# Performance work log

Hardware: AMD Instinct MI355X
Metric: run time of the kernel (lower is better)

The kernel has to match this reference:

```python
import jax, jax.numpy as jnp
import numpy as np

B, T, HID = 2, 2048, 1024
H, D = 16, 64
ROPE = 32
GIDX = (2, 3, 4, 5)
MASK_VAL = -1e9


def setup_inputs() -> dict:
    key = jax.random.key(0)
    ks = jax.random.split(key, 5)
    x = jax.random.normal(ks[0], (B, T, HID), jnp.float32)
    mask = jnp.triu(jnp.ones((T, T), jnp.bool_), 1)  # True above diagonal -> masked (causal)
    qkv_w = jax.random.normal(ks[1], (3 * H * D, HID), jnp.float32) * (1.0 / np.sqrt(HID))
    qkv_b = jax.random.normal(ks[2], (3 * H * D,), jnp.float32) * 0.02
    out_w = jax.random.normal(ks[3], (HID, H * D), jnp.float32) * (1.0 / np.sqrt(H * D))
    out_b = jax.random.normal(ks[4], (HID,), jnp.float32) * 0.02
    return {"x": x, "mask": mask, "qkv_w": qkv_w, "qkv_b": qkv_b, "out_w": out_w, "out_b": out_b}


def _rope_tables(t):
    inv_freq = 1.0 / (10000.0 ** (jnp.arange(0, ROPE, 2, dtype=jnp.float32) / ROPE))
    freqs = jnp.arange(t, dtype=jnp.float32)[:, None] * inv_freq[None, :]  # [T, ROPE/2]
    return jnp.cos(freqs), jnp.sin(freqs)


def _apply_rotary(x, cos, sin):
    # x: [B,H,T,D]; rotate first ROPE dims as interleaved pairs
    xr = x[..., :ROPE].reshape(*x.shape[:-1], ROPE // 2, 2)
    x1, x2 = xr[..., 0], xr[..., 1]
    rot = jnp.stack([x1 * cos - x2 * sin, x1 * sin + x2 * cos], axis=-1).reshape(*x.shape[:-1], ROPE)
    return jnp.concatenate([rot, x[..., ROPE:]], axis=-1)


def reference(x, mask, qkv_w, qkv_b, out_w, out_b):
    b, t, _ = x.shape
    qkv = x @ qkv_w.T + qkv_b                      # [B,T,3*H*D]
    q, k, v = jnp.split(qkv, 3, axis=-1)
    q, k, v = [y.reshape(b, t, H, D).transpose(0, 2, 1, 3) for y in (q, k, v)]  # [B,H,T,D]
    cos, sin = _rope_tables(t)                      # [T, ROPE/2] broadcast over B,H
    q = _apply_rotary(q, cos, sin)
    k = _apply_rotary(k, cos, sin)
    scale = 1.0 / np.sqrt(D)
    # local dense causal attention
    scores = jnp.einsum('bhqd,bhkd->bhqk', q, k) * scale
    scores = jnp.where(mask, MASK_VAL, scores)
    out_local = jnp.einsum('bhqk,bhkd->bhqd', jax.nn.softmax(scores, axis=-1), v)
    # global token pass with its own causal overlay
    gidx = jnp.array(GIDX)
    gq = q[:, :, gidx]                              # [B,H,G,D]
    gs = jnp.einsum('bhgd,bhkd->bhgk', gq, k) * scale
    gmask = jnp.arange(t)[None, :] > gidx[:, None]  # [G,T]: col > row -> masked
    gs = jnp.where(gmask, MASK_VAL, gs)
    gout = jnp.einsum('bhgk,bhkd->bhgd', jax.nn.softmax(gs, axis=-1), v)
    out = out_local.at[:, :, gidx].set(gout)
    attn_out = out.transpose(0, 2, 1, 3).reshape(b, t, H * D)
    return attn_out @ out_w.T + out_b
```

## Files before the change

### kernel.cpp

```cpp
#include <hip/hip_runtime.h>
#include <math.h>

typedef unsigned short u16;
typedef unsigned int u32;
typedef __attribute__((ext_vector_type(4))) float f32x4;
typedef __attribute__((ext_vector_type(8))) short bf16x8;

#define B_ 2
#define T_ 2048
#define H_ 16
#define HID 1024
#define NQKV 3072
#define M_ 4096
#define SCALE_Q 0.18033688011112042f

__device__ __forceinline__ u16 f2bf(float f) {
  union { float f; unsigned u; } v; v.f = f;
  unsigned r = v.u + 0x7FFFu + ((v.u >> 16) & 1u);
  return (u16)(r >> 16);
}
__device__ __forceinline__ float bf2f(u16 u) {
  union { unsigned u; float f; } v; v.u = ((unsigned)u) << 16; return v.f;
}
__device__ __forceinline__ u32 cvt_pk_bf16(float lo, float hi) {
  u32 r;
  asm("v_cvt_pk_bf16_f32 %0, %1, %2" : "=v"(r) : "v"(lo), "v"(hi));
  return r;
}
__device__ __forceinline__ float fexp2(float x) { return __builtin_amdgcn_exp2f(x); }

__device__ __forceinline__ void gload16(const void* g, void* l) {
  __builtin_amdgcn_global_load_lds((const __attribute__((address_space(1))) void*)g,
                                   (__attribute__((address_space(3))) void*)l, 16, 0, 0);
}

__global__ void prep(const float* __restrict__ x, const float* __restrict__ qkv_w,
                     const float* __restrict__ out_w, u16* __restrict__ xb,
                     u16* __restrict__ wqkv, u16* __restrict__ wout, float* __restrict__ tab) {
  int bid = blockIdx.x;
  if (bid < 128) {
    int i = bid * 256 + threadIdx.x;
    int tpos = i >> 4, f = i & 15;
    float ang = (float)tpos * exp2f(-(float)f * 0.83048202372184058696f);
    float s, c;
    sincosf(ang, &s, &c);
    tab[i * 2] = c;
    tab[i * 2 + 1] = s;
    return;
  }
  bid -= 128;
  const float* in;
  u16* out;
  if (bid < 4096) { in = x; out = xb; }
  else if (bid < 7168) { bid -= 4096; in = qkv_w; out = wqkv; }
  else { bid -= 7168; in = out_w; out = wout; }
  int i = bid * 256 + threadIdx.x;
  float4 v = ((const float4*)in)[i];
  uint2 o;
  o.x = (unsigned)f2bf(v.x) | ((unsigned)f2bf(v.y) << 16);
  o.y = (unsigned)f2bf(v.z) | ((unsigned)f2bf(v.w) << 16);
  ((uint2*)out)[i] = o;
}

__global__ __launch_bounds__(256) void gemm_qkv(const u16* __restrict__ A,
    const u16* __restrict__ Bt, const float* __restrict__ bias, const float* __restrict__ tab,
    u16* __restrict__ Q, u16* __restrict__ K, u16* __restrict__ Vt)
{
  __shared__ u16 lsA[2][128 * 32];
  __shared__ u16 lsB[2][128 * 32];
  const int t = threadIdx.x;
  const int l = t & 63, w = t >> 6;
  const int wm = (w >> 1) * 64, wn = (w & 1) * 64;
  const int lr = l & 15, lg = l >> 4;
  const long bm = (long)blockIdx.y * 128, bn = (long)blockIdx.x * 128;
  const int KD = HID;

  f32x4 acc[4][4];
#pragma unroll
  for (int i = 0; i < 4; i++)
#pragma unroll
    for (int j = 0; j < 4; j++) acc[i][j] = (f32x4){0.f, 0.f, 0.f, 0.f};

  const int srow = l >> 2, sko = (l & 3) * 8;
  const u16* Ab = A + (bm + srow) * (long)KD + sko;
  const u16* Bb = Bt + (bn + srow) * (long)KD + sko;

  auto stage = [&](int buf, int k0) {
#pragma unroll
    for (int g = 0; g < 2; g++)
      gload16(Ab + (long)((w * 2 + g) * 16) * KD + k0, &lsA[buf][(w * 2 + g) * 512]);
#pragma unroll
    for (int g = 0; g < 2; g++)
      gload16(Bb + (long)((w * 2 + g) * 16) * KD + k0, &lsB[buf][(w * 2 + g) * 512]);
  };

  stage(0, 0);
  __syncthreads();
  int cur = 0;
  for (int k0 = 0; k0 < KD; k0 += 32) {
    if (k0 + 32 < KD) stage(cur ^ 1, k0 + 32);
    bf16x8 af[4], bfv[4];
#pragma unroll
    for (int mi = 0; mi < 4; mi++)
      af[mi] = *(const bf16x8*)&lsA[cur][(wm + mi * 16 + lr) * 32 + lg * 8];
#pragma unroll
    for (int ni = 0; ni < 4; ni++)
      bfv[ni] = *(const bf16x8*)&lsB[cur][(wn + ni * 16 + lr) * 32 + lg * 8];
    __builtin_amdgcn_s_setprio(1);
#pragma unroll
    for (int mi = 0; mi < 4; mi++)
#pragma unroll
      for (int ni = 0; ni < 4; ni++)
        acc[mi][ni] = __builtin_amdgcn_mfma_f32_16x16x32_bf16(af[mi], bfv[ni], acc[mi][ni], 0, 0, 0);
    __builtin_amdgcn_s_setprio(0);
    __syncthreads();
    cur ^= 1;
  }

  const int region = (int)(bn >> 10);
  const int h = (int)(((bn + wn) & 1023) >> 6);
  const float2* tab2 = (const float2*)tab;
  u16* QK = (region == 0) ? Q : K;

#pragma unroll
  for (int mi = 0; mi < 4; mi++) {
    const int m0 = (int)(bm) + wm + mi * 16 + lg * 4;
    const int b = m0 >> 11, t0 = m0 & (T_ - 1);
    const long bh = b * 16 + h;
#pragma unroll
    for (int ni = 0; ni < 4; ni++) {
      const int d = ni * 16 + lr;
      const long col = bn + wn + d;
      const float bv = bias[col];
      float vv[4];
#pragma unroll
      for (int r = 0; r < 4; r++) vv[r] = acc[mi][ni][r] + bv;
      if (region < 2 && ni < 2) {
        const int fi = d >> 1;
        const float sgn = (d & 1) ? 1.f : -1.f;
#pragma unroll
        for (int r = 0; r < 4; r++) {
          float pvv = __shfl_xor(vv[r], 1, 64);
          float2 cs = tab2[(t0 + r) * 16 + fi];
          vv[r] = vv[r] * cs.x + sgn * pvv * cs.y;
        }
      }
      if (region == 0) {
#pragma unroll
        for (int r = 0; r < 4; r++) vv[r] *= SCALE_Q;
      }
      if (region < 2) {
#pragma unroll
        for (int r = 0; r < 4; r++)
          QK[(bh * T_ + t0 + r) * 64 + d] = f2bf(vv[r]);
      } else {
        uint2 pk;
        pk.x = cvt_pk_bf16(vv[0], vv[1]);
        pk.y = cvt_pk_bf16(vv[2], vv[3]);
        *(uint2*)&Vt[(bh * 64 + d) * (long)T_ + t0] = pk;
      }
    }
  }
}

__global__ __launch_bounds__(256) void gemm_out(const u16* __restrict__ A,
    const u16* __restrict__ Bt, const float* __restrict__ bias,
    float* __restrict__ outp, int N, int K)
{
  constexpr int BM = 64;
  constexpr int MI = 4, NI = 2;
  __shared__ u16 lsA[2][BM * 32];
  __shared__ u16 lsB[2][128 * 32];
  const int t = threadIdx.x;
  const int l = t & 63, w = t >> 6;
  const int wn = w * 32;
  const int lr = l & 15, lg = l >> 4;
  const long bm = (long)blockIdx.y * BM, bn = (long)blockIdx.x * 128;

  f32x4 acc[MI][NI];
#pragma unroll
  for (int i = 0; i < MI; i++)
#pragma unroll
    for (int j = 0; j < NI; j++) acc[i][j] = (f32x4){0.f, 0.f, 0.f, 0.f};

  const int srow = l >> 2, sko = (l & 3) * 8;
  const u16* Ab = A + (bm + srow) * (long)K + sko;
  const u16* Bb = Bt + (bn + srow) * (long)K + sko;

  auto stage = [&](int buf, int k0) {
    gload16(Ab + (long)(w * 16) * K + k0, &lsA[buf][w * 512]);
    gload16(Bb + (long)(w * 16) * K + k0, &lsB[buf][w * 512]);
    gload16(Bb + (long)((w + 4) * 16) * K + k0, &lsB[buf][(w + 4) * 512]);
  };

  stage(0, 0);
  __syncthreads();
  int cur = 0;
  for (int k0 = 0; k0 < K; k0 += 32) {
    if (k0 + 32 < K) stage(cur ^ 1, k0 + 32);
    bf16x8 af[MI], bfv[NI];
#pragma unroll
    for (int mi = 0; mi < MI; mi++)
      af[mi] = *(const bf16x8*)&lsA[cur][(mi * 16 + lr) * 32 + lg * 8];
#pragma unroll
    for (int ni = 0; ni < NI; ni++)
      bfv[ni] = *(const bf16x8*)&lsB[cur][(wn + ni * 16 + lr) * 32 + lg * 8];
    __builtin_amdgcn_s_setprio(1);
#pragma unroll
    for (int mi = 0; mi < MI; mi++)
#pragma unroll
      for (int ni = 0; ni < NI; ni++)
        acc[mi][ni] = __builtin_amdgcn_mfma_f32_16x16x32_bf16(af[mi], bfv[ni], acc[mi][ni], 0, 0, 0);
    __builtin_amdgcn_s_setprio(0);
    __syncthreads();
    cur ^= 1;
  }
#pragma unroll
  for (int mi = 0; mi < MI; mi++)
#pragma unroll
    for (int ni = 0; ni < NI; ni++) {
      long row = bm + mi * 16 + lg * 4;
      long col = bn + wn + ni * 16 + lr;
      float bv = bias[col];
#pragma unroll
      for (int r = 0; r < 4; r++)
        outp[(row + r) * (long)N + col] = acc[mi][ni][r] + bv;
    }
}

__global__ __launch_bounds__(256, 4) void fattn(const u16* __restrict__ Q, const u16* __restrict__ Kp,
                                                const u16* __restrict__ V, u16* __restrict__ O) {
  const int id = blockIdx.x;
  const int qt = 31 - (id >> 5);
  const int bh = id & 31;
  __shared__ u16 lsK[2][64 * 64];
  __shared__ u16 lsV[2][64 * 64];
  __shared__ u32 lsP[4][16 * 36];
  const int t = threadIdx.x, l = t & 63, w = t >> 6;
  const int lr = l & 15, lg = l >> 4;
  const u16* Qb = Q + (long)bh * T_ * 64;
  const u16* Kb = Kp + (long)bh * T_ * 64;
  const u16* Vb = V + (long)bh * 64 * T_;
  u32* lsPw = lsP[w];

  bf16x8 aq[2];
#pragma unroll
  for (int ks = 0; ks < 2; ks++)
    aq[ks] = *(const bf16x8*)&Qb[((long)(qt * 64 + w * 16 + lr)) * 64 + ks * 32 + lg * 8];

  f32x4 o[4];
#pragma unroll
  for (int di = 0; di < 4; di++) o[di] = (f32x4){0.f, 0.f, 0.f, 0.f};
  float mrow = -1e30f, lrow = 0.f;

  const int srow = l >> 3;
  const int scx = ((l & 7) ^ srow) * 8;
  const long kgo0 = (long)(16 * w + srow) * 64 + scx;
  const long kgo1 = (long)(16 * w + 8 + srow) * 64 + scx;
  const long vgo0 = (long)(16 * w + srow) * T_ + scx;
  const long vgo1 = (long)(16 * w + 8 + srow) * T_ + scx;

  gload16(Kb + kgo0, &lsK[0][(2 * w) * 512]);
  gload16(Kb + kgo1, &lsK[0][(2 * w + 1) * 512]);
  gload16(Vb + vgo0, &lsV[0][(2 * w) * 512]);
  gload16(Vb + vgo1, &lsV[0][(2 * w + 1) * 512]);
  __syncthreads();

  int cur = 0;
  for (int kt = 0; kt <= qt; kt++) {
    if (kt < qt) {
      const u16* kp = Kb + (kt + 1) * 4096;
      const u16* vp = Vb + (kt + 1) * 64;
      gload16(kp + kgo0, &lsK[cur ^ 1][(2 * w) * 512]);
      gload16(kp + kgo1, &lsK[cur ^ 1][(2 * w + 1) * 512]);
      gload16(vp + vgo0, &lsV[cur ^ 1][(2 * w) * 512]);
      gload16(vp + vgo1, &lsV[cur ^ 1][(2 * w + 1) * 512]);
    }

    f32x4 s[4];
#pragma unroll
    for (int ji = 0; ji < 4; ji++) s[ji] = (f32x4){0.f, 0.f, 0.f, 0.f};
    __builtin_amdgcn_s_setprio(1);
#pragma unroll
    for (int ks = 0; ks < 2; ks++)
#pragma unroll
      for (int ji = 0; ji < 4; ji++) {
        int row = ji * 16 + lr;
        bf16x8 kf = *(const bf16x8*)&lsK[cur][row * 64 + ((ks * 32 + lg * 8) ^ ((row & 7) * 8))];
        s[ji] = __builtin_amdgcn_mfma_f32_16x16x32_bf16(kf, aq[ks], s[ji], 0, 0, 0);
      }
    __builtin_amdgcn_s_setprio(0);

    if (kt == qt) {
      int qloc = w * 16 + lr;
#pragma unroll
      for (int ji = 0; ji < 4; ji++)
#pragma unroll
        for (int r = 0; r < 4; r++)
          if (ji * 16 + lg * 4 + r > qloc) s[ji][r] = -1e30f;
    }

    float mx = s[0][0];
#pragma unroll
    for (int ji = 0; ji < 4; ji++)
#pragma unroll
      for (int r = 0; r < 4; r++) mx = fmaxf(mx, s[ji][r]);
    mx = fmaxf(mx, __shfl_xor(mx, 16, 64));
    mx = fmaxf(mx, __shfl_xor(mx, 32, 64));

    if (__any(mx - mrow > 8.f)) {
      float newm = fmaxf(mrow, mx);
      float sf = fexp2(mrow - newm);
      mrow = newm;
      lrow *= sf;
#pragma unroll
      for (int r = 0; r < 4; r++) {
        float sfb = __shfl(sf, lg * 4 + r, 64);
#pragma unroll
        for (int di = 0; di < 4; di++) o[di][r] *= sfb;
      }
    }

    float rs = 0.f;
    u32 pd[8];
#pragma unroll
    for (int ji = 0; ji < 4; ji++)
#pragma unroll
      for (int hh = 0; hh < 2; hh++) {
        float p0 = fexp2(s[ji][2 * hh] - mrow);
        float p1 = fexp2(s[ji][2 * hh + 1] - mrow);
        rs += p0 + p1;
        pd[ji * 2 + hh] = cvt_pk_bf16(p0, p1);
      }
    rs += __shfl_xor(rs, 16, 64);
    rs += __shfl_xor(rs, 32, 64);
    lrow += rs;

#pragma unroll
    for (int ji = 0; ji < 4; ji++)
      *(uint2*)&lsPw[lr * 36 + ji * 8 + lg * 2] = make_uint2(pd[2 * ji], pd[2 * ji + 1]);
    __builtin_amdgcn_s_setprio(1);
#pragma unroll
    for (int js = 0; js < 2; js++) {
      bf16x8 pa = *(const bf16x8*)&lsPw[lr * 36 + js * 16 + lg * 4];
#pragma unroll
      for (int di = 0; di < 4; di++) {
        int drow = di * 16 + lr;
        bf16x8 vb = *(const bf16x8*)&lsV[cur][drow * 64 + ((js * 32 + lg * 8) ^ ((drow & 7) * 8))];
        o[di] = __builtin_amdgcn_mfma_f32_16x16x32_bf16(pa, vb, o[di], 0, 0, 0);
      }
    }
    __builtin_amdgcn_s_setprio(0);

    if (kt < qt) __syncthreads();
    cur ^= 1;
  }

  const int b = bh >> 4, h = bh & 15;
  float inv = 1.f / lrow;
#pragma unroll
  for (int r = 0; r < 4; r++) {
    float invb = __shfl(inv, lg * 4 + r, 64);
#pragma unroll
    for (int di = 0; di < 4; di++) {
      long rowt = (long)(b * T_ + qt * 64 + w * 16 + lg * 4 + r);
      O[rowt * 1024 + h * 64 + di * 16 + lr] = f2bf(o[di][r] * invb);
    }
  }
}

extern "C" void kernel_launch(void* const* d_in, const int* in_sizes, int n_in,
                              void* d_out, int out_size, void* d_ws, size_t ws_size,
                              hipStream_t stream) {
  (void)in_sizes; (void)n_in; (void)out_size; (void)ws_size;
  const float* x     = (const float*)d_in[0];
  const float* qkv_w = (const float*)d_in[2];
  const float* qkv_b = (const float*)d_in[3];
  const float* out_w = (const float*)d_in[4];
  const float* out_b = (const float*)d_in[5];
  char* ws = (char*)d_ws;
  size_t off = 0;
  auto alloc = [&](size_t n) { void* p = ws + off; off += (n + 255) & ~(size_t)255; return p; };
  u16*   xb    = (u16*)alloc((size_t)M_ * HID * 2);
  u16*   wqkv  = (u16*)alloc((size_t)NQKV * HID * 2);
  u16*   wout  = (u16*)alloc((size_t)HID * HID * 2);
  u16*   Qb    = (u16*)alloc((size_t)M_ * HID * 2);
  u16*   Kb    = (u16*)alloc((size_t)M_ * HID * 2);
  u16*   Vtb   = (u16*)alloc((size_t)M_ * HID * 2);
  u16*   attnb = (u16*)alloc((size_t)M_ * HID * 2);
  float* tab   = (float*)alloc((size_t)T_ * 16 * 2 * 4);

  prep<<<8320, 256, 0, stream>>>(x, qkv_w, out_w, xb, wqkv, wout, tab);
  gemm_qkv<<<dim3(NQKV / 128, M_ / 128), 256, 0, stream>>>(xb, wqkv, qkv_b, tab, Qb, Kb, Vtb);
  fattn<<<1024, 256, 0, stream>>>(Qb, Kb, Vtb, attnb);
  gemm_out<<<dim3(HID / 128, M_ / 64), 256, 0, stream>>>(attnb, wout, out_b, (float*)d_out, HID, HID);
}
```

Measured before the change: 194.3 us.

## Rewrite flash attention with 32x32x16 MFMA and register-resident P via permlane swap

The attention kernel now uses 2 waves per block, each owning 32 query rows, and computes QK^T and PV with 32x32x16 bf16 MFMAs in place of 16x16x32. The softmax probabilities are repacked into the MFMA operand layout in registers with v_permlane32_swap, which removes the LDS round trip for P and its shared buffer. Row max and sum reductions mostly happen within a lane because of the transposed score layout. The cost is fewer threads per block, more accumulator registers per wave, and each thread issuing four K/V staging loads instead of two.

```diff
diff --git a/kernel.cpp b/kernel.cpp
--- a/kernel.cpp
+++ b/kernel.cpp
@@ -4,6 +4,7 @@
 typedef unsigned short u16;
 typedef unsigned int u32;
 typedef __attribute__((ext_vector_type(4))) float f32x4;
+typedef __attribute__((ext_vector_type(16))) float f32x16;
 typedef __attribute__((ext_vector_type(8))) short bf16x8;
 
 #define B_ 2
@@ -26,6 +27,9 @@
   u32 r;
   asm("v_cvt_pk_bf16_f32 %0, %1, %2" : "=v"(r) : "v"(lo), "v"(hi));
   return r;
+}
+__device__ __forceinline__ void perm32swap(u32& a, u32& b) {
+  asm volatile("v_permlane32_swap_b32 %0, %1" : "+v"(a), "+v"(b));
 }
 __device__ __forceinline__ float fexp2(float x) { return __builtin_amdgcn_exp2f(x); }
 
@@ -228,84 +232,92 @@
     }
 }
 
-__global__ __launch_bounds__(256, 4) void fattn(const u16* __restrict__ Q, const u16* __restrict__ Kp,
+__global__ __launch_bounds__(128, 2) void fattn(const u16* __restrict__ Q, const u16* __restrict__ Kp,
                                                 const u16* __restrict__ V, u16* __restrict__ O) {
   const int id = blockIdx.x;
-  const int qt = 31 - (id >> 5);
+  const int qs = 31 - (id >> 5);
   const int bh = id & 31;
   __shared__ u16 lsK[2][64 * 64];
   __shared__ u16 lsV[2][64 * 64];
-  __shared__ u32 lsP[4][16 * 36];
   const int t = threadIdx.x, l = t & 63, w = t >> 6;
-  const int lr = l & 15, lg = l >> 4;
+  const int lq = l & 31, hi = l >> 5;
   const u16* Qb = Q + (long)bh * T_ * 64;
   const u16* Kb = Kp + (long)bh * T_ * 64;
   const u16* Vb = V + (long)bh * 64 * T_;
-  u32* lsPw = lsP[w];
-
-  bf16x8 aq[2];
-#pragma unroll
-  for (int ks = 0; ks < 2; ks++)
-    aq[ks] = *(const bf16x8*)&Qb[((long)(qt * 64 + w * 16 + lr)) * 64 + ks * 32 + lg * 8];
-
-  f32x4 o[4];
-#pragma unroll
-  for (int di = 0; di < 4; di++) o[di] = (f32x4){0.f, 0.f, 0.f, 0.f};
+  const int qbase = qs * 64 + w * 32;
+  const int qg = qbase + lq;
+
+  bf16x8 aq[4];
+#pragma unroll
+  for (int ds = 0; ds < 4; ds++)
+    aq[ds] = *(const bf16x8*)&Qb[(long)qg * 64 + ds * 16 + hi * 8];
+
+  f32x16 oac[2];
+#pragma unroll
+  for (int d0 = 0; d0 < 2; d0++)
+#pragma unroll
+    for (int i = 0; i < 16; i++) oac[d0][i] = 0.f;
   float mrow = -1e30f, lrow = 0.f;
 
   const int srow = l >> 3;
   const int scx = ((l & 7) ^ srow) * 8;
-  const long kgo0 = (long)(16 * w + srow) * 64 + scx;
-  const long kgo1 = (long)(16 * w + 8 + srow) * 64 + scx;
-  const long vgo0 = (long)(16 * w + srow) * T_ + scx;
-  const long vgo1 = (long)(16 * w + 8 + srow) * T_ + scx;
-
-  gload16(Kb + kgo0, &lsK[0][(2 * w) * 512]);
-  gload16(Kb + kgo1, &lsK[0][(2 * w + 1) * 512]);
-  gload16(Vb + vgo0, &lsV[0][(2 * w) * 512]);
-  gload16(Vb + vgo1, &lsV[0][(2 * w + 1) * 512]);
+  long kgo[4], vgo[4];
+#pragma unroll
+  for (int g = 0; g < 4; g++) {
+    kgo[g] = (long)(32 * w + 8 * g + srow) * 64 + scx;
+    vgo[g] = (long)(32 * w + 8 * g + srow) * T_ + scx;
+  }
+  auto stage = [&](int buf, const u16* kp, const u16* vp) {
+#pragma unroll
+    for (int g = 0; g < 4; g++) {
+      gload16(kp + kgo[g], &lsK[buf][(4 * w + g) * 512]);
+      gload16(vp + vgo[g], &lsV[buf][(4 * w + g) * 512]);
+    }
+  };
+
+  stage(0, Kb, Vb);
   __syncthreads();
 
   int cur = 0;
-  for (int kt = 0; kt <= qt; kt++) {
-    if (kt < qt) {
-      const u16* kp = Kb + (kt + 1) * 4096;
-      const u16* vp = Vb + (kt + 1) * 64;
-      gload16(kp + kgo0, &lsK[cur ^ 1][(2 * w) * 512]);
-      gload16(kp + kgo1, &lsK[cur ^ 1][(2 * w + 1) * 512]);
-      gload16(vp + vgo0, &lsV[cur ^ 1][(2 * w) * 512]);
-      gload16(vp + vgo1, &lsV[cur ^ 1][(2 * w + 1) * 512]);
-    }
-
-    f32x4 s[4];
-#pragma unroll
-    for (int ji = 0; ji < 4; ji++) s[ji] = (f32x4){0.f, 0.f, 0.f, 0.f};
+  for (int kt = 0; kt <= qs; kt++) {
+    if (kt < qs)
+      stage(cur ^ 1, Kb + (long)(kt + 1) * 4096, Vb + (long)(kt + 1) * 64);
+
+    f32x16 s2[2];
+#pragma unroll
+    for (int ks2 = 0; ks2 < 2; ks2++)
+#pragma unroll
+      for (int i = 0; i < 16; i++) s2[ks2][i] = 0.f;
     __builtin_amdgcn_s_setprio(1);
 #pragma unroll
-    for (int ks = 0; ks < 2; ks++)
-#pragma unroll
-      for (int ji = 0; ji < 4; ji++) {
-        int row = ji * 16 + lr;
-        bf16x8 kf = *(const bf16x8*)&lsK[cur][row * 64 + ((ks * 32 + lg * 8) ^ ((row & 7) * 8))];
-        s[ji] = __builtin_amdgcn_mfma_f32_16x16x32_bf16(kf, aq[ks], s[ji], 0, 0, 0);
+    for (int ds = 0; ds < 4; ds++)
+#pragma unroll
+      for (int ks2 = 0; ks2 < 2; ks2++) {
+        int arow = ks2 * 32 + lq;
+        bf16x8 kf = *(const bf16x8*)&lsK[cur][arow * 64 + ((ds * 16 + hi * 8) ^ ((arow & 7) * 8))];
+        s2[ks2] = __builtin_amdgcn_mfma_f32_32x32x16_bf16(kf, aq[ds], s2[ks2], 0, 0, 0);
       }
     __builtin_amdgcn_s_setprio(0);
 
-    if (kt == qt) {
-      int qloc = w * 16 + lr;
-#pragma unroll
-      for (int ji = 0; ji < 4; ji++)
-#pragma unroll
-        for (int r = 0; r < 4; r++)
-          if (ji * 16 + lg * 4 + r > qloc) s[ji][r] = -1e30f;
-    }
-
-    float mx = s[0][0];
-#pragma unroll
-    for (int ji = 0; ji < 4; ji++)
-#pragma unroll
-      for (int r = 0; r < 4; r++) mx = fmaxf(mx, s[ji][r]);
-    mx = fmaxf(mx, __shfl_xor(mx, 16, 64));
+    if (kt == qs) {
+      const int kbase = kt * 64;
+#pragma unroll
+      for (int ks2 = 0; ks2 < 2; ks2++)
+#pragma unroll
+        for (int rg = 0; rg < 16; rg++) {
+          int kglob = kbase + ks2 * 32 + (rg & 3) + 8 * (rg >> 2) + 4 * hi;
+          if (kglob > qg) s2[ks2][rg] = -1e30f;
+        }
+    }
+
+    float tv[16];
+#pragma unroll
+    for (int i = 0; i < 16; i++) tv[i] = fmaxf(s2[0][i], s2[1][i]);
+#pragma unroll
+    for (int i = 0; i < 8; i++) tv[i] = fmaxf(tv[i], tv[i + 8]);
+#pragma unroll
+    for (int i = 0; i < 4; i++) tv[i] = fmaxf(tv[i], tv[i + 4]);
+    float mx = fmaxf(fmaxf(tv[0], tv[1]), fmaxf(tv[2], tv[3]));
     mx = fmaxf(mx, __shfl_xor(mx, 32, 64));
 
     if (__any(mx - mrow > 8.f)) {
@@ -314,59 +326,73 @@
       mrow = newm;
       lrow *= sf;
 #pragma unroll
-      for (int r = 0; r < 4; r++) {
-        float sfb = __shfl(sf, lg * 4 + r, 64);
-#pragma unroll
-        for (int di = 0; di < 4; di++) o[di][r] *= sfb;
-      }
-    }
-
-    float rs = 0.f;
-    u32 pd[8];
-#pragma unroll
-    for (int ji = 0; ji < 4; ji++)
-#pragma unroll
-      for (int hh = 0; hh < 2; hh++) {
-        float p0 = fexp2(s[ji][2 * hh] - mrow);
-        float p1 = fexp2(s[ji][2 * hh + 1] - mrow);
-        rs += p0 + p1;
-        pd[ji * 2 + hh] = cvt_pk_bf16(p0, p1);
-      }
-    rs += __shfl_xor(rs, 16, 64);
+      for (int d0 = 0; d0 < 2; d0++)
+#pragma unroll
+        for (int i = 0; i < 16; i++) oac[d0][i] *= sf;
+    }
+
+    float pv[32];
+#pragma unroll
+    for (int ks2 = 0; ks2 < 2; ks2++)
+#pragma unroll
+      for (int rg = 0; rg < 16; rg++) pv[ks2 * 16 + rg] = fexp2(s2[ks2][rg] - mrow);
+
+    float sv[16];
+#pragma unroll
+    for (int i = 0; i < 16; i++) sv[i] = pv[i] + pv[i + 16];
+#pragma unroll
+    for (int i = 0; i < 8; i++) sv[i] = sv[i] + sv[i + 8];
+#pragma unroll
+    for (int i = 0; i < 4; i++) sv[i] = sv[i] + sv[i + 4];
+    float rs = (sv[0] + sv[1]) + (sv[2] + sv[3]);
     rs += __shfl_xor(rs, 32, 64);
     lrow += rs;
 
-#pragma unroll
-    for (int ji = 0; ji < 4; ji++)
-      *(uint2*)&lsPw[lr * 36 + ji * 8 + lg * 2] = make_uint2(pd[2 * ji], pd[2 * ji + 1]);
+    bf16x8 pf[2][2];
+#pragma unroll
+    for (int ks2 = 0; ks2 < 2; ks2++)
+#pragma unroll
+      for (int s = 0; s < 2; s++) {
+        u32 a0 = cvt_pk_bf16(pv[ks2 * 16 + 8 * s + 0], pv[ks2 * 16 + 8 * s + 1]);
+        u32 b0 = cvt_pk_bf16(pv[ks2 * 16 + 8 * s + 4], pv[ks2 * 16 + 8 * s + 5]);
+        u32 a1 = cvt_pk_bf16(pv[ks2 * 16 + 8 * s + 2], pv[ks2 * 16 + 8 * s + 3]);
+        u32 b1 = cvt_pk_bf16(pv[ks2 * 16 + 8 * s + 6], pv[ks2 * 16 + 8 * s + 7]);
+        perm32swap(a0, b0);
+        perm32swap(a1, b1);
+        uint4 fr = make_uint4(a0, a1, b0, b1);
+        pf[ks2][s] = *(bf16x8*)&fr;
+      }
+
     __builtin_amdgcn_s_setprio(1);
 #pragma unroll
-    for (int js = 0; js < 2; js++) {
-      bf16x8 pa = *(const bf16x8*)&lsPw[lr * 36 + js * 16 + lg * 4];
-#pragma unroll
-      for (int di = 0; di < 4; di++) {
-        int drow = di * 16 + lr;
-        bf16x8 vb = *(const bf16x8*)&lsV[cur][drow * 64 + ((js * 32 + lg * 8) ^ ((drow & 7) * 8))];
-        o[di] = __builtin_amdgcn_mfma_f32_16x16x32_bf16(pa, vb, o[di], 0, 0, 0);
-      }
-    }
+    for (int d0 = 0; d0 < 2; d0++)
+#pragma unroll
+      for (int ks2 = 0; ks2 < 2; ks2++)
+#pragma unroll
+        for (int s = 0; s < 2; s++) {
+          int arow = d0 * 32 + lq;
+          bf16x8 vb = *(const bf16x8*)&lsV[cur][arow * 64 +
+                          ((ks2 * 32 + s * 16 + hi * 8) ^ ((arow & 7) * 8))];
+          oac[d0] = __builtin_amdgcn_mfma_f32_32x32x16_bf16(vb, pf[ks2][s], oac[d0], 0, 0, 0);
+        }
     __builtin_amdgcn_s_setprio(0);
 
-    if (kt < qt) __syncthreads();
+    if (kt < qs) __syncthreads();
     cur ^= 1;
   }
 
   const int b = bh >> 4, h = bh & 15;
-  float inv = 1.f / lrow;
-#pragma unroll
-  for (int r = 0; r < 4; r++) {
-    float invb = __shfl(inv, lg * 4 + r, 64);
-#pragma unroll
-    for (int di = 0; di < 4; di++) {
-      long rowt = (long)(b * T_ + qt * 64 + w * 16 + lg * 4 + r);
-      O[rowt * 1024 + h * 64 + di * 16 + lr] = f2bf(o[di][r] * invb);
-    }
-  }
+  const float inv = 1.f / lrow;
+  u16* obase = O + ((long)(b * T_ + qg)) * 1024 + h * 64;
+#pragma unroll
+  for (int d0 = 0; d0 < 2; d0++)
+#pragma unroll
+    for (int rp = 0; rp < 8; rp++) {
+      int rg = rp * 2;
+      int d = d0 * 32 + (rg & 3) + 8 * (rg >> 2) + 4 * hi;
+      u32 pk = cvt_pk_bf16(oac[d0][rg] * inv, oac[d0][rg + 1] * inv);
+      *(u32*)&obase[d] = pk;
+    }
 }
 
 extern "C" void kernel_launch(void* const* d_in, const int* in_sizes, int n_in,
@@ -392,6 +418,6 @@
 
   prep<<<8320, 256, 0, stream>>>(x, qkv_w, out_w, xb, wqkv, wout, tab);
   gemm_qkv<<<dim3(NQKV / 128, M_ / 128), 256, 0, stream>>>(xb, wqkv, qkv_b, tab, Qb, Kb, Vtb);
-  fattn<<<1024, 256, 0, stream>>>(Qb, Kb, Vtb, attnb);
+  fattn<<<1024, 128, 0, stream>>>(Qb, Kb, Vtb, attnb);
   gemm_out<<<dim3(HID / 128, M_ / 64), 256, 0, stream>>>(attnb, wout, out_b, (float*)d_out, HID, HID);
 }
```

Result: no change. 197.7 us (+1.7%).
